# Kernel optimization log

Measured on AMD Instinct MI355X. Metric: run time of the kernel, lower is better.

The kernel has to match this reference:

```python
import jax, jax.numpy as jnp
import numpy as np

N_A = N_B = N_C = 50000
E = 800000
D_IN = 256
D_OUT = 128
T_ATT = 64


def _spmm(row, col, val, ft, n_dst):
    # sparse [n_dst, n_src] @ ft : gather src rows, scale, scatter-add to dst
    return jax.ops.segment_sum(val[:, None] * ft[col], row, num_segments=n_dst)


def setup_inputs() -> dict:
    key = jax.random.key(0)
    ks = jax.random.split(key, 40)
    f32 = jnp.float32
    inp = {
        'x_a': jax.random.normal(ks[0], (N_A, D_IN), f32),
        'x_b': jax.random.normal(ks[1], (N_B, D_IN), f32),
        'x_c': jax.random.normal(ks[2], (N_C, D_IN), f32),
    }
    # COO adjacency per relation: (dst_row, src_col, value)
    rel = {'ab': (N_A, N_B), 'ac': (N_A, N_C), 'ba': (N_B, N_A), 'ca': (N_C, N_A)}
    i = 3
    for name, (nd, ns) in rel.items():
        inp['row_' + name] = jax.random.randint(ks[i], (E,), 0, nd); i += 1
        inp['col_' + name] = jax.random.randint(ks[i], (E,), 0, ns); i += 1
        inp['val_' + name] = jax.random.uniform(ks[i], (E,), f32); i += 1
    # learned parameters (xavier-ish scale)
    def w(k, shape, s=0.05):
        return jax.random.normal(k, shape, f32) * s
    inp['w_self_a'] = w(ks[i], (D_IN, D_OUT)); i += 1
    inp['w_self_b'] = w(ks[i], (D_IN, D_OUT)); i += 1
    inp['w_self_c'] = w(ks[i], (D_IN, D_OUT)); i += 1
    inp['W_ab'] = w(ks[i], (D_IN, D_OUT)); i += 1
    inp['W_ac'] = w(ks[i], (D_IN, D_OUT)); i += 1
    inp['W_ba'] = w(ks[i], (D_IN, D_OUT)); i += 1
    inp['W_ca'] = w(ks[i], (D_IN, D_OUT)); i += 1
    inp['bias_a'] = w(ks[i], (1, D_OUT)); i += 1
    inp['bias_b'] = w(ks[i], (1, D_OUT)); i += 1
    inp['bias_c'] = w(ks[i], (1, D_OUT)); i += 1
    inp['w_cat_a'] = w(ks[i], (2 * D_OUT, D_OUT)); i += 1
    inp['w_cat_b'] = w(ks[i], (2 * D_OUT, D_OUT)); i += 1
    inp['w_cat_c'] = w(ks[i], (2 * D_OUT, D_OUT)); i += 1
    inp['w_query_a'] = w(ks[i], (D_OUT, T_ATT)); i += 1
    inp['w_keys_a'] = w(ks[i], (D_OUT, T_ATT)); i += 1
    inp['w_att_a'] = w(ks[i], (2 * T_ATT, 1)); i += 1
    return inp


def reference(x_a, x_b, x_c,
              row_ab, col_ab, val_ab, row_ac, col_ac, val_ac,
              row_ba, col_ba, val_ba, row_ca, col_ca, val_ca,
              w_self_a, w_self_b, w_self_c,
              W_ab, W_ac, W_ba, W_ca,
              bias_a, bias_b, bias_c,
              w_cat_a, w_cat_b, w_cat_c,
              w_query_a, w_keys_a, w_att_a):
    # ---- type 'a': neighbors [b, c], attention fusion ----
    self_a = x_a @ w_self_a                                   # [Na, D]
    nb_b = _spmm(row_ab, col_ab, val_ab, x_b @ W_ab, N_A)     # [Na, D]
    nb_c = _spmm(row_ac, col_ac, val_ac, x_c @ W_ac, N_A)     # [Na, D]
    q = self_a @ w_query_a                                    # [Na, T]
    e_b = jax.nn.elu(jnp.concatenate([nb_b @ w_keys_a, q], 1) @ w_att_a)  # [Na, 1]
    e_c = jax.nn.elu(jnp.concatenate([nb_c @ w_keys_a, q], 1) @ w_att_a)  # [Na, 1]
    att = jax.nn.softmax(jnp.concatenate([e_b, e_c], 1), axis=1)          # [Na, 2]
    agg_a = nb_b * att[:, :1] + nb_c * att[:, 1:2]
    out_a = jnp.concatenate([agg_a, self_a], 1) @ w_cat_a + bias_a
    # ---- type 'b': single neighbor 'a' ----
    self_b = x_b @ w_self_b
    agg_b = _spmm(row_ba, col_ba, val_ba, x_a @ W_ba, N_B)
    out_b = jnp.concatenate([agg_b, self_b], 1) @ w_cat_b + bias_b
    # ---- type 'c': single neighbor 'a' ----
    self_c = x_c @ w_self_c
    agg_c = _spmm(row_ca, col_ca, val_ca, x_a @ W_ca, N_C)
    out_c = jnp.concatenate([agg_c, self_c], 1) @ w_cat_c + bias_c
    # concat per-type outputs (all D_OUT wide) into one array
    return jnp.concatenate([out_a, out_b, out_c], 0)          # [Na+Nb+Nc, D]
```

## Files before the change

kernel.cpp:

```cpp
#include <hip/hip_runtime.h>

#define NA 50000
#define NE 800000
#define NBKT 196
#define CAP 4608
#define BSTRIDE (NBKT * CAP)

typedef unsigned int   u32;
typedef unsigned short u16;
typedef short s16x8 __attribute__((ext_vector_type(8)));
typedef float f32x4 __attribute__((ext_vector_type(4)));

__device__ __forceinline__ u16 f2bf(float f) {
  u32 u = __float_as_uint(f);
  u += 0x7fffu + ((u >> 16) & 1u);
  return (u16)(u >> 16);
}

__device__ __forceinline__ void acc8(float* a, uint4 q, float v) {
  a[0] += v * __uint_as_float(q.x << 16);
  a[1] += v * __uint_as_float(q.x & 0xffff0000u);
  a[2] += v * __uint_as_float(q.y << 16);
  a[3] += v * __uint_as_float(q.y & 0xffff0000u);
  a[4] += v * __uint_as_float(q.z << 16);
  a[5] += v * __uint_as_float(q.z & 0xffff0000u);
  a[6] += v * __uint_as_float(q.w << 16);
  a[7] += v * __uint_as_float(q.w & 0xffff0000u);
}

struct Rel4 { const int* row[4]; const int* col[4]; const float* val[4]; };

struct Prep {
  const float* src[10]; u16* dst[10];
  const float* wq; const float* wk; const float* wa; float* uvp;
  u32* gcur;
};

struct ConvArgs { const float* x[3]; u16* xb; };

struct FtArgs { const u16* A[3]; const u16* Bt[3]; u16* C[3]; };

__global__ __launch_bounds__(256) void k_prep(Prep P) {
  int gy = blockIdx.y;
  if (gy < 10) {
    int idx = blockIdx.x * 256 + threadIdx.x;
    int k = idx & 255, n = idx >> 8;
    P.dst[gy][n * 256 + k] = f2bf(P.src[gy][k * 128 + n]);
  } else if (blockIdx.x == 0) {
    int t = threadIdx.x;
    int d = t & 127, which = t >> 7;
    const float* w = which ? P.wq : P.wk;
    const float* a = P.wa + which * 64;
    float s = 0.f;
    for (int i = 0; i < 64; ++i) s += w[d * 64 + i] * a[i];
    P.uvp[which * 128 + d] = s;
  } else if (blockIdx.x == 1) {
    for (int i = threadIdx.x; i < 1024; i += 256)
      P.gcur[i] = (u32)((i & 255) * CAP);
  }
}

__global__ __launch_bounds__(256) void k_main1(Rel4 R, u32* __restrict__ gcur,
                                               uint2* __restrict__ pairs, ConvArgs CA) {
  __shared__ __align__(16) char smem[40960];
  const int gy = blockIdx.y;
  const int t = threadIdx.x;
  if (gy < 4) {
    if (blockIdx.x >= 196) return;
    int rel = gy;
    int e0 = blockIdx.x * 4096;
    int nrem = min(4096, NE - e0);
    u32* sw0  = (u32*)smem;
    u32* sval = sw0 + 4096;
    unsigned char* sbkt = (unsigned char*)(sval + 4096);
    u32* hist  = (u32*)(sbkt + 4096);
    u32* lscan = hist + 256;
    u32* cnt2  = lscan + 256;
    u32* gbase = cnt2 + 256;
    hist[t] = 0; cnt2[t] = 0;
    __syncthreads();
    const int* rr = R.row[rel];
    const int* cc = R.col[rel];
    const float* vl = R.val[rel];
    u32 w0[16]; u32 vv[16]; int bb[16];
    #pragma unroll
    for (int i = 0; i < 16; ++i) {
      int li = t + i * 256;
      bool ok = li < nrem;
      int idx = e0 + (ok ? li : 0);
      int r = ok ? rr[idx] : 0;
      int c = ok ? cc[idx] : 0;
      float v = ok ? vl[idx] : 0.f;
      u32 b = (u32)r >> 8;
      w0[i] = (u32)(c & 0xFFFF) | ((u32)(r & 255) << 16) | (b << 24);
      vv[i] = __float_as_uint(v);
      bb[i] = ok ? (int)b : -1;
      if (ok) atomicAdd(&hist[b], 1u);
    }
    __syncthreads();
    lscan[t] = hist[t];
    __syncthreads();
    for (int ofs = 1; ofs < 256; ofs <<= 1) {
      u32 y = (t >= ofs) ? lscan[t - ofs] : 0u;
      __syncthreads();
      lscan[t] += y;
      __syncthreads();
    }
    gbase[t] = atomicAdd(&gcur[rel * 256 + t], hist[t]);
    #pragma unroll
    for (int i = 0; i < 16; ++i) {
      if (bb[i] >= 0) {
        int b = bb[i];
        u32 p = (lscan[b] - hist[b]) + atomicAdd(&cnt2[b], 1u);
        sw0[p] = w0[i]; sval[p] = vv[i]; sbkt[p] = (unsigned char)b;
      }
    }
    __syncthreads();
    uint2* P = pairs + (size_t)rel * BSTRIDE;
    #pragma unroll
    for (int i = 0; i < 16; ++i) {
      int p = t + i * 256;
      if (p < nrem) {
        int b = sbkt[p];
        u32 gd = gbase[b] + (u32)p - (lscan[b] - hist[b]);
        uint2 pr; pr.x = sw0[p]; pr.y = sval[p];
        P[gd] = pr;
      }
    }
  } else {
    const size_t TOT = 38400000;
    const size_t TSZ = 12800000;
    size_t base = ((size_t)(gy - 4) * 391 + blockIdx.x) * 16384 + (size_t)t * 8;
    #pragma unroll
    for (int it = 0; it < 8; ++it) {
      size_t g = base + (size_t)it * 2048;
      if (g < TOT) {
        int which = (g >= 2 * TSZ) ? 2 : (g >= TSZ ? 1 : 0);
        size_t off = g - (size_t)which * TSZ;
        const float* sp = CA.x[which] + off;
        float4 v0 = *(const float4*)(sp);
        float4 v1 = *(const float4*)(sp + 4);
        s16x8 o;
        o[0] = (short)f2bf(v0.x); o[1] = (short)f2bf(v0.y);
        o[2] = (short)f2bf(v0.z); o[3] = (short)f2bf(v0.w);
        o[4] = (short)f2bf(v1.x); o[5] = (short)f2bf(v1.y);
        o[6] = (short)f2bf(v1.z); o[7] = (short)f2bf(v1.w);
        *(s16x8*)(CA.xb + g) = o;
      }
    }
  }
}

__global__ __launch_bounds__(256) void k_main2(const u32* __restrict__ gcur,
    int* __restrict__ ofs_s, int* __restrict__ ofs_e,
    const uint2* __restrict__ pairs, u32* __restrict__ epak, FtArgs Ar) {
  __shared__ __align__(16) char smem[40960];
  const int gy = blockIdx.y;
  const int t = threadIdx.x;
  if (gy < 4) {
    if (blockIdx.x >= 196) return;
    int rel = gy;
    int b = blockIdx.x;
    int base = b * CAP;
    int n = (int)gcur[rel * 256 + b] - base;
    u32* sw0  = (u32*)smem;
    u32* sv   = sw0 + CAP;
    u32* hist = sv + CAP;
    u32* scan = hist + 256;
    u32* cur  = scan + 256;
    hist[t] = 0;
    __syncthreads();
    const uint2* P = pairs + (size_t)rel * BSTRIDE;
    for (int p = t; p < n; p += 256) {
      uint2 pr = P[base + p];
      sw0[p] = pr.x; sv[p] = pr.y;
      atomicAdd(&hist[(pr.x >> 16) & 255], 1u);
    }
    __syncthreads();
    u32 own = hist[t];
    scan[t] = own;
    __syncthreads();
    for (int ofs = 1; ofs < 256; ofs <<= 1) {
      u32 y = (t >= ofs) ? scan[t - ofs] : 0u;
      __syncthreads();
      scan[t] += y;
      __syncthreads();
    }
    u32 excl = scan[t] - own;
    cur[t] = excl;
    int r0 = b << 8;
    if (r0 + t < NA) {
      ofs_s[(size_t)rel * NA + r0 + t] = base + (int)excl;
      ofs_e[(size_t)rel * NA + r0 + t] = base + (int)(excl + own);
    }
    __syncthreads();
    u32* E = epak + (size_t)rel * BSTRIDE;
    for (int p = t; p < n; p += 256) {
      u32 w = sw0[p];
      int rl = (w >> 16) & 255;
      u32 d = atomicAdd(&cur[rl], 1u);
      E[base + (int)d] = (w & 0xFFFFu) | ((u32)f2bf(__uint_as_float(sv[p])) << 16);
    }
  } else {
    u16* Al = (u16*)smem;
    u16* Bl = Al + 128 * 72;
    const int by = gy - 4;
    const int which = (by < 3) ? 0 : (by < 5 ? 1 : 2);
    const int col0 = (by - (which == 0 ? 0 : (which == 1 ? 3 : 5))) * 128;
    const int ldc = (which == 0) ? 384 : 256;
    const u16* A = Ar.A[which];
    const u16* Bt = Ar.Bt[which] + (size_t)col0 * 256;
    u16* C = Ar.C[which] + col0;
    const int row0 = blockIdx.x * 128;
    const int w = t >> 6, l = t & 63;
    const int wr = (w >> 1) * 64, wc = (w & 1) * 64;
    const int sr = t >> 1, kb = (t & 1) * 32;
    f32x4 acc[4][4] = {};
    for (int kk = 0; kk < 4; ++kk) {
      if (row0 + sr < NA) {
        const u16* ap = A + (size_t)(row0 + sr) * 256 + kk * 64 + kb;
        #pragma unroll
        for (int h = 0; h < 4; ++h)
          *(s16x8*)&Al[sr * 72 + kb + h * 8] = *(const s16x8*)(ap + h * 8);
      } else {
        s16x8 z = {0,0,0,0,0,0,0,0};
        #pragma unroll
        for (int h = 0; h < 4; ++h) *(s16x8*)&Al[sr * 72 + kb + h * 8] = z;
      }
      {
        const u16* bp = Bt + (size_t)sr * 256 + kk * 64 + kb;
        #pragma unroll
        for (int h = 0; h < 4; ++h)
          *(s16x8*)&Bl[sr * 72 + kb + h * 8] = *(const s16x8*)(bp + h * 8);
      }
      __syncthreads();
      #pragma unroll
      for (int ks = 0; ks < 2; ++ks) {
        s16x8 af[4], bfr[4];
        #pragma unroll
        for (int i = 0; i < 4; ++i)
          af[i] = *(const s16x8*)&Al[(wr + i * 16 + (l & 15)) * 72 + ks * 32 + (l >> 4) * 8];
        #pragma unroll
        for (int j = 0; j < 4; ++j)
          bfr[j] = *(const s16x8*)&Bl[(wc + j * 16 + (l & 15)) * 72 + ks * 32 + (l >> 4) * 8];
        #pragma unroll
        for (int i = 0; i < 4; ++i)
          #pragma unroll
          for (int j = 0; j < 4; ++j)
            acc[i][j] = __builtin_amdgcn_mfma_f32_16x16x32_bf16(af[i], bfr[j], acc[i][j], 0, 0, 0);
      }
      __syncthreads();
    }
    #pragma unroll
    for (int i = 0; i < 4; ++i)
      #pragma unroll
      for (int j = 0; j < 4; ++j)
        #pragma unroll
        for (int q = 0; q < 4; ++q) {
          int r = row0 + wr + i * 16 + (l >> 4) * 4 + q;
          if (r < NA) C[(size_t)r * ldc + wc + j * 16 + (l & 15)] = f2bf(acc[i][j][q]);
        }
  }
}

__global__ __launch_bounds__(256) void k_spmm(
    const int* __restrict__ ofs_s, const int* __restrict__ ofs_e,
    const u32* __restrict__ epak,
    const u16* __restrict__ ya, const u16* __restrict__ yb, const u16* __restrict__ yc,
    const float* __restrict__ uv,
    u16* __restrict__ agg_a, u16* __restrict__ agg_b, u16* __restrict__ agg_c) {
  int tid = threadIdx.x;
  int lane = tid & 63, wid = tid >> 6;
  int g = lane >> 4, gl = lane & 15;
  int row = blockIdx.x * 16 + wid * 4 + g;
  int gy = blockIdx.y;
  if (gy == 0) {
    float fb[8] = {0,0,0,0,0,0,0,0};
    float fc[8] = {0,0,0,0,0,0,0,0};
    {
      const u32* pr = epak;
      int i = ofs_s[row], e = ofs_e[row];
      for (; i + 4 <= e; i += 4) {
        u32 p0 = pr[i], p1 = pr[i + 1], p2 = pr[i + 2], p3 = pr[i + 3];
        uint4 q0 = *(const uint4*)((const u32*)(yb + (size_t)(p0 & 0xFFFFu) * 256) + gl * 4);
        uint4 q1 = *(const uint4*)((const u32*)(yb + (size_t)(p1 & 0xFFFFu) * 256) + gl * 4);
        uint4 q2 = *(const uint4*)((const u32*)(yb + (size_t)(p2 & 0xFFFFu) * 256) + gl * 4);
        uint4 q3 = *(const uint4*)((const u32*)(yb + (size_t)(p3 & 0xFFFFu) * 256) + gl * 4);
        acc8(fb, q0, __uint_as_float(p0 & 0xffff0000u));
        acc8(fb, q1, __uint_as_float(p1 & 0xffff0000u));
        acc8(fb, q2, __uint_as_float(p2 & 0xffff0000u));
        acc8(fb, q3, __uint_as_float(p3 & 0xffff0000u));
      }
      for (; i < e; ++i) {
        u32 p0 = pr[i];
        uint4 q0 = *(const uint4*)((const u32*)(yb + (size_t)(p0 & 0xFFFFu) * 256) + gl * 4);
        acc8(fb, q0, __uint_as_float(p0 & 0xffff0000u));
      }
    }
    {
      const u32* pr = epak + (size_t)BSTRIDE;
      int i = ofs_s[NA + row], e = ofs_e[NA + row];
      for (; i + 4 <= e; i += 4) {
        u32 p0 = pr[i], p1 = pr[i + 1], p2 = pr[i + 2], p3 = pr[i + 3];
        uint4 q0 = *(const uint4*)((const u32*)(yc + (size_t)(p0 & 0xFFFFu) * 256) + gl * 4);
        uint4 q1 = *(const uint4*)((const u32*)(yc + (size_t)(p1 & 0xFFFFu) * 256) + gl * 4);
        uint4 q2 = *(const uint4*)((const u32*)(yc + (size_t)(p2 & 0xFFFFu) * 256) + gl * 4);
        uint4 q3 = *(const uint4*)((const u32*)(yc + (size_t)(p3 & 0xFFFFu) * 256) + gl * 4);
        acc8(fc, q0, __uint_as_float(p0 & 0xffff0000u));
        acc8(fc, q1, __uint_as_float(p1 & 0xffff0000u));
        acc8(fc, q2, __uint_as_float(p2 & 0xffff0000u));
        acc8(fc, q3, __uint_as_float(p3 & 0xffff0000u));
      }
      for (; i < e; ++i) {
        u32 p0 = pr[i];
        uint4 q0 = *(const uint4*)((const u32*)(yc + (size_t)(p0 & 0xFFFFu) * 256) + gl * 4);
        acc8(fc, q0, __uint_as_float(p0 & 0xffff0000u));
      }
    }
    float sf[8];
    {
      uint4 sq = *(const uint4*)((const u32*)(ya + (size_t)row * 384) + gl * 4);
      sf[0] = __uint_as_float(sq.x << 16); sf[1] = __uint_as_float(sq.x & 0xffff0000u);
      sf[2] = __uint_as_float(sq.y << 16); sf[3] = __uint_as_float(sq.y & 0xffff0000u);
      sf[4] = __uint_as_float(sq.z << 16); sf[5] = __uint_as_float(sq.z & 0xffff0000u);
      sf[6] = __uint_as_float(sq.w << 16); sf[7] = __uint_as_float(sq.w & 0xffff0000u);
    }
    float pb = 0.f, pc = 0.f, pq = 0.f;
    const float* up = uv + gl * 8;
    const float* vp = uv + 128 + gl * 8;
    #pragma unroll
    for (int j = 0; j < 8; ++j) {
      pb += fb[j] * up[j];
      pc += fc[j] * up[j];
      pq += sf[j] * vp[j];
    }
    #pragma unroll
    for (int off = 1; off < 16; off <<= 1) {
      pb += __shfl_xor(pb, off);
      pc += __shfl_xor(pc, off);
      pq += __shfl_xor(pq, off);
    }
    float eb = pb + pq, ec = pc + pq;
    eb = eb > 0.f ? eb : (expf(eb) - 1.f);
    ec = ec > 0.f ? ec : (expf(ec) - 1.f);
    float m = fmaxf(eb, ec);
    float p0 = expf(eb - m), p1 = expf(ec - m);
    float inv = 1.f / (p0 + p1);
    float a0 = p0 * inv, a1 = p1 * inv;
    uint4 o;
    o.x = (u32)f2bf(a0 * fb[0] + a1 * fc[0]) | ((u32)f2bf(a0 * fb[1] + a1 * fc[1]) << 16);
    o.y = (u32)f2bf(a0 * fb[2] + a1 * fc[2]) | ((u32)f2bf(a0 * fb[3] + a1 * fc[3]) << 16);
    o.z = (u32)f2bf(a0 * fb[4] + a1 * fc[4]) | ((u32)f2bf(a0 * fb[5] + a1 * fc[5]) << 16);
    o.w = (u32)f2bf(a0 * fb[6] + a1 * fc[6]) | ((u32)f2bf(a0 * fb[7] + a1 * fc[7]) << 16);
    *(uint4*)((u32*)(agg_a + (size_t)row * 128) + gl * 4) = o;
  } else {
    int which = gy - 1;
    const int* os = ofs_s + (2 + which) * NA;
    const int* oe = ofs_e + (2 + which) * NA;
    const u32* pr = epak + (size_t)(2 + which) * BSTRIDE;
    const u16* ft = ya + (which ? 256 : 128);
    u16* agg = which ? agg_c : agg_b;
    float fa[8] = {0,0,0,0,0,0,0,0};
    int i = os[row], e = oe[row];
    for (; i + 4 <= e; i += 4) {
      u32 p0 = pr[i], p1 = pr[i + 1], p2 = pr[i + 2], p3 = pr[i + 3];
      uint4 q0 = *(const uint4*)((const u32*)(ft + (size_t)(p0 & 0xFFFFu) * 384) + gl * 4);
      uint4 q1 = *(const uint4*)((const u32*)(ft + (size_t)(p1 & 0xFFFFu) * 384) + gl * 4);
      uint4 q2 = *(const uint4*)((const u32*)(ft + (size_t)(p2 & 0xFFFFu) * 384) + gl * 4);
      uint4 q3 = *(const uint4*)((const u32*)(ft + (size_t)(p3 & 0xFFFFu) * 384) + gl * 4);
      acc8(fa, q0, __uint_as_float(p0 & 0xffff0000u));
      acc8(fa, q1, __uint_as_float(p1 & 0xffff0000u));
      acc8(fa, q2, __uint_as_float(p2 & 0xffff0000u));
      acc8(fa, q3, __uint_as_float(p3 & 0xffff0000u));
    }
    for (; i < e; ++i) {
      u32 p0 = pr[i];
      uint4 q0 = *(const uint4*)((const u32*)(ft + (size_t)(p0 & 0xFFFFu) * 384) + gl * 4);
      acc8(fa, q0, __uint_as_float(p0 & 0xffff0000u));
    }
    uint4 o;
    o.x = (u32)f2bf(fa[0]) | ((u32)f2bf(fa[1]) << 16);
    o.y = (u32)f2bf(fa[2]) | ((u32)f2bf(fa[3]) << 16);
    o.z = (u32)f2bf(fa[4]) | ((u32)f2bf(fa[5]) << 16);
    o.w = (u32)f2bf(fa[6]) | ((u32)f2bf(fa[7]) << 16);
    *(uint4*)((u32*)(agg + (size_t)row * 128) + gl * 4) = o;
  }
}

struct OutArgs {
  const u16* Agg[3]; const u16* Self[3]; int lds_[3];
  const u16* Bt[3]; const float* bias[3]; float* Out[3];
};

__global__ __launch_bounds__(256) void k_gemm_out(OutArgs Ar) {
  __shared__ u16 Al[128 * 72];
  __shared__ u16 Bl[128 * 72];
  const int which = blockIdx.y;
  const u16* Agg = Ar.Agg[which];
  const u16* Self = Ar.Self[which];
  const int ldself = Ar.lds_[which];
  const u16* Bt = Ar.Bt[which];
  const float* bias = Ar.bias[which];
  float* Out = Ar.Out[which];
  const int row0 = blockIdx.x * 128;
  const int t = threadIdx.x;
  const int w = t >> 6, l = t & 63;
  const int wr = (w >> 1) * 64, wc = (w & 1) * 64;
  const int sr = t >> 1, kb = (t & 1) * 32;
  f32x4 acc[4][4] = {};
  for (int kk = 0; kk < 4; ++kk) {
    {
      const u16* sp = (kk < 2) ? (Agg + (size_t)(row0 + sr) * 128 + kk * 64 + kb)
                               : (Self + (size_t)(row0 + sr) * ldself + (kk - 2) * 64 + kb);
      if (row0 + sr < NA) {
        #pragma unroll
        for (int h = 0; h < 4; ++h)
          *(s16x8*)&Al[sr * 72 + kb + h * 8] = *(const s16x8*)(sp + h * 8);
      } else {
        s16x8 z = {0,0,0,0,0,0,0,0};
        #pragma unroll
        for (int h = 0; h < 4; ++h) *(s16x8*)&Al[sr * 72 + kb + h * 8] = z;
      }
    }
    {
      const u16* bp = Bt + (size_t)sr * 256 + kk * 64 + kb;
      #pragma unroll
      for (int h = 0; h < 4; ++h)
        *(s16x8*)&Bl[sr * 72 + kb + h * 8] = *(const s16x8*)(bp + h * 8);
    }
    __syncthreads();
    #pragma unroll
    for (int ks = 0; ks < 2; ++ks) {
      s16x8 af[4], bfr[4];
      #pragma unroll
      for (int i = 0; i < 4; ++i)
        af[i] = *(const s16x8*)&Al[(wr + i * 16 + (l & 15)) * 72 + ks * 32 + (l >> 4) * 8];
      #pragma unroll
      for (int j = 0; j < 4; ++j)
        bfr[j] = *(const s16x8*)&Bl[(wc + j * 16 + (l & 15)) * 72 + ks * 32 + (l >> 4) * 8];
      #pragma unroll
      for (int i = 0; i < 4; ++i)
        #pragma unroll
        for (int j = 0; j < 4; ++j)
          acc[i][j] = __builtin_amdgcn_mfma_f32_16x16x32_bf16(af[i], bfr[j], acc[i][j], 0, 0, 0);
    }
    __syncthreads();
  }
  #pragma unroll
  for (int i = 0; i < 4; ++i)
    #pragma unroll
    for (int j = 0; j < 4; ++j)
      #pragma unroll
      for (int q = 0; q < 4; ++q) {
        int r = row0 + wr + i * 16 + (l >> 4) * 4 + q;
        int c = wc + j * 16 + (l & 15);
        if (r < NA) Out[(size_t)r * 128 + c] = acc[i][j][q] + bias[c];
      }
}

extern "C" void kernel_launch(void* const* d_in, const int* in_sizes, int n_in,
                              void* d_out, int out_size, void* d_ws, size_t ws_size,
                              hipStream_t stream) {
  const float* x_a = (const float*)d_in[0];
  const float* x_b = (const float*)d_in[1];
  const float* x_c = (const float*)d_in[2];
  const int* row_ab = (const int*)d_in[3];
  const int* col_ab = (const int*)d_in[4];
  const float* val_ab = (const float*)d_in[5];
  const int* row_ac = (const int*)d_in[6];
  const int* col_ac = (const int*)d_in[7];
  const float* val_ac = (const float*)d_in[8];
  const int* row_ba = (const int*)d_in[9];
  const int* col_ba = (const int*)d_in[10];
  const float* val_ba = (const float*)d_in[11];
  const int* row_ca = (const int*)d_in[12];
  const int* col_ca = (const int*)d_in[13];
  const float* val_ca = (const float*)d_in[14];
  const float* w_self_a = (const float*)d_in[15];
  const float* w_self_b = (const float*)d_in[16];
  const float* w_self_c = (const float*)d_in[17];
  const float* W_ab = (const float*)d_in[18];
  const float* W_ac = (const float*)d_in[19];
  const float* W_ba = (const float*)d_in[20];
  const float* W_ca = (const float*)d_in[21];
  const float* bias_a = (const float*)d_in[22];
  const float* bias_b = (const float*)d_in[23];
  const float* bias_c = (const float*)d_in[24];
  const float* w_cat_a = (const float*)d_in[25];
  const float* w_cat_b = (const float*)d_in[26];
  const float* w_cat_c = (const float*)d_in[27];
  const float* w_query_a = (const float*)d_in[28];
  const float* w_keys_a = (const float*)d_in[29];
  const float* w_att_a = (const float*)d_in[30];

  float* out = (float*)d_out;

  char* ws = (char*)d_ws;
  size_t off_b = 0;
  auto walloc = [&](size_t bytes) {
    void* p = ws + off_b;
    off_b = (off_b + bytes + 255) & ~(size_t)255;
    return p;
  };
  u16* ya = (u16*)walloc((size_t)NA * 384 * 2);
  u16* yb = (u16*)walloc((size_t)NA * 256 * 2);
  u16* yc = (u16*)walloc((size_t)NA * 256 * 2);
  u16* agg_a = (u16*)walloc((size_t)NA * 128 * 2);
  u16* agg_b = (u16*)walloc((size_t)NA * 128 * 2);
  u16* agg_c = (u16*)walloc((size_t)NA * 128 * 2);
  int* ofs_s = (int*)walloc((size_t)4 * NA * 4);
  int* ofs_e = (int*)walloc((size_t)4 * NA * 4);
  u32* gcur = (u32*)walloc((size_t)4 * 256 * 4);
  uint2* pairs = (uint2*)walloc((size_t)4 * BSTRIDE * 8);
  u32* epak = (u32*)walloc((size_t)4 * BSTRIDE * 4);
  u16* Wa_t = (u16*)walloc((size_t)384 * 256 * 2);
  u16* Wb_t = (u16*)walloc((size_t)256 * 256 * 2);
  u16* Wc_t = (u16*)walloc((size_t)256 * 256 * 2);
  u16* Wcat_a = (u16*)walloc((size_t)128 * 256 * 2);
  u16* Wcat_b = (u16*)walloc((size_t)128 * 256 * 2);
  u16* Wcat_c = (u16*)walloc((size_t)128 * 256 * 2);
  float* uvbuf = (float*)walloc(256 * 4);
  u16* xb = (u16*)walloc((size_t)3 * NA * 256 * 2);

  Rel4 R;
  R.row[0] = row_ab; R.col[0] = col_ab; R.val[0] = val_ab;
  R.row[1] = row_ac; R.col[1] = col_ac; R.val[1] = val_ac;
  R.row[2] = row_ba; R.col[2] = col_ba; R.val[2] = val_ba;
  R.row[3] = row_ca; R.col[3] = col_ca; R.val[3] = val_ca;

  Prep P;
  P.src[0] = w_self_a; P.dst[0] = Wa_t;
  P.src[1] = W_ba;     P.dst[1] = Wa_t + 128 * 256;
  P.src[2] = W_ca;     P.dst[2] = Wa_t + 256 * 256;
  P.src[3] = W_ab;     P.dst[3] = Wb_t;
  P.src[4] = w_self_b; P.dst[4] = Wb_t + 128 * 256;
  P.src[5] = W_ac;     P.dst[5] = Wc_t;
  P.src[6] = w_self_c; P.dst[6] = Wc_t + 128 * 256;
  P.src[7] = w_cat_a;  P.dst[7] = Wcat_a;
  P.src[8] = w_cat_b;  P.dst[8] = Wcat_b;
  P.src[9] = w_cat_c;  P.dst[9] = Wcat_c;
  P.wq = w_query_a; P.wk = w_keys_a; P.wa = w_att_a; P.uvp = uvbuf;
  P.gcur = gcur;

  dim3 gp(128, 11);
  k_prep<<<gp, 256, 0, stream>>>(P);

  ConvArgs CA;
  CA.x[0] = x_a; CA.x[1] = x_b; CA.x[2] = x_c;
  CA.xb = xb;
  dim3 g1(391, 11);
  k_main1<<<g1, 256, 0, stream>>>(R, gcur, pairs, CA);

  FtArgs FA;
  FA.A[0] = xb; FA.A[1] = xb + (size_t)NA * 256; FA.A[2] = xb + (size_t)2 * NA * 256;
  FA.Bt[0] = Wa_t; FA.Bt[1] = Wb_t; FA.Bt[2] = Wc_t;
  FA.C[0] = ya; FA.C[1] = yb; FA.C[2] = yc;
  dim3 g2(391, 11);
  k_main2<<<g2, 256, 0, stream>>>(gcur, ofs_s, ofs_e, pairs, epak, FA);

  dim3 gs(3125, 3);
  k_spmm<<<gs, 256, 0, stream>>>(ofs_s, ofs_e, epak, ya, yb, yc, uvbuf,
                                 agg_a, agg_b, agg_c);

  OutArgs OA;
  OA.Agg[0] = agg_a; OA.Agg[1] = agg_b; OA.Agg[2] = agg_c;
  OA.Self[0] = ya; OA.Self[1] = yb + 128; OA.Self[2] = yc + 128;
  OA.lds_[0] = 384; OA.lds_[1] = 256; OA.lds_[2] = 256;
  OA.Bt[0] = Wcat_a; OA.Bt[1] = Wcat_b; OA.Bt[2] = Wcat_c;
  OA.bias[0] = bias_a; OA.bias[1] = bias_b; OA.bias[2] = bias_c;
  OA.Out[0] = out; OA.Out[1] = out + (size_t)NA * 128; OA.Out[2] = out + (size_t)NA * 128 * 2;
  dim3 go(391, 3);
  k_gemm_out<<<go, 256, 0, stream>>>(OA);
}
```

Measured before the change: 308.3 us.

## Fuse output concat-GEMM into SpMM epilogue with MFMA-fragment weight layout

The final concat+linear GEMM is folded into the SpMM kernel. Each block stages its 16 aggregated rows plus the matching self features in LDS, then runs a small MFMA GEMM against w_cat, with the weights pre-laid out in fragment order during prep. This removes the agg buffers, one kernel launch, and the round trip through global memory. In exchange each SpMM block does extra work, and the weight fragments are reloaded from global or L2 for every block.

```diff
diff --git a/kernel.cpp b/kernel.cpp
--- a/kernel.cpp
+++ b/kernel.cpp
@@ -40,12 +40,20 @@
 
 struct FtArgs { const u16* A[3]; const u16* Bt[3]; u16* C[3]; };
 
+struct FuseW { const u16* Wf[3]; const float* bias[3]; float* out[3]; };
+
 __global__ __launch_bounds__(256) void k_prep(Prep P) {
   int gy = blockIdx.y;
-  if (gy < 10) {
+  if (gy < 7) {
     int idx = blockIdx.x * 256 + threadIdx.x;
     int k = idx & 255, n = idx >> 8;
     P.dst[gy][n * 256 + k] = f2bf(P.src[gy][k * 128 + n]);
+  } else if (gy < 10) {
+    int idx = blockIdx.x * 256 + threadIdx.x;
+    int e = idx & 7, l = (idx >> 3) & 63, jj = (idx >> 9) & 7, ks = idx >> 12;
+    int n = jj * 16 + (l & 15);
+    int k = ks * 32 + ((l >> 4) * 8) + e;
+    P.dst[gy][idx] = f2bf(P.src[gy][k * 128 + n]);
   } else if (blockIdx.x == 0) {
     int t = threadIdx.x;
     int d = t & 127, which = t >> 7;
@@ -267,12 +275,13 @@
     const int* __restrict__ ofs_s, const int* __restrict__ ofs_e,
     const u32* __restrict__ epak,
     const u16* __restrict__ ya, const u16* __restrict__ yb, const u16* __restrict__ yc,
-    const float* __restrict__ uv,
-    u16* __restrict__ agg_a, u16* __restrict__ agg_b, u16* __restrict__ agg_c) {
+    const float* __restrict__ uv, FuseW FW) {
+  __shared__ u16 Asm[16 * 264];
   int tid = threadIdx.x;
   int lane = tid & 63, wid = tid >> 6;
   int g = lane >> 4, gl = lane & 15;
-  int row = blockIdx.x * 16 + wid * 4 + g;
+  int lr = wid * 4 + g;
+  int row = blockIdx.x * 16 + lr;
   int gy = blockIdx.y;
   if (gy == 0) {
     float fb[8] = {0,0,0,0,0,0,0,0};
@@ -317,14 +326,12 @@
         acc8(fc, q0, __uint_as_float(p0 & 0xffff0000u));
       }
     }
+    uint4 sq = *(const uint4*)((const u32*)(ya + (size_t)row * 384) + gl * 4);
     float sf[8];
-    {
-      uint4 sq = *(const uint4*)((const u32*)(ya + (size_t)row * 384) + gl * 4);
-      sf[0] = __uint_as_float(sq.x << 16); sf[1] = __uint_as_float(sq.x & 0xffff0000u);
-      sf[2] = __uint_as_float(sq.y << 16); sf[3] = __uint_as_float(sq.y & 0xffff0000u);
-      sf[4] = __uint_as_float(sq.z << 16); sf[5] = __uint_as_float(sq.z & 0xffff0000u);
-      sf[6] = __uint_as_float(sq.w << 16); sf[7] = __uint_as_float(sq.w & 0xffff0000u);
-    }
+    sf[0] = __uint_as_float(sq.x << 16); sf[1] = __uint_as_float(sq.x & 0xffff0000u);
+    sf[2] = __uint_as_float(sq.y << 16); sf[3] = __uint_as_float(sq.y & 0xffff0000u);
+    sf[4] = __uint_as_float(sq.z << 16); sf[5] = __uint_as_float(sq.z & 0xffff0000u);
+    sf[6] = __uint_as_float(sq.w << 16); sf[7] = __uint_as_float(sq.w & 0xffff0000u);
     float pb = 0.f, pc = 0.f, pq = 0.f;
     const float* up = uv + gl * 8;
     const float* vp = uv + 128 + gl * 8;
@@ -347,19 +354,18 @@
     float p0 = expf(eb - m), p1 = expf(ec - m);
     float inv = 1.f / (p0 + p1);
     float a0 = p0 * inv, a1 = p1 * inv;
-    uint4 o;
-    o.x = (u32)f2bf(a0 * fb[0] + a1 * fc[0]) | ((u32)f2bf(a0 * fb[1] + a1 * fc[1]) << 16);
-    o.y = (u32)f2bf(a0 * fb[2] + a1 * fc[2]) | ((u32)f2bf(a0 * fb[3] + a1 * fc[3]) << 16);
-    o.z = (u32)f2bf(a0 * fb[4] + a1 * fc[4]) | ((u32)f2bf(a0 * fb[5] + a1 * fc[5]) << 16);
-    o.w = (u32)f2bf(a0 * fb[6] + a1 * fc[6]) | ((u32)f2bf(a0 * fb[7] + a1 * fc[7]) << 16);
-    *(uint4*)((u32*)(agg_a + (size_t)row * 128) + gl * 4) = o;
+    s16x8 av;
+    #pragma unroll
+    for (int j = 0; j < 8; ++j) av[j] = (short)f2bf(a0 * fb[j] + a1 * fc[j]);
+    *(s16x8*)&Asm[lr * 264 + gl * 8] = av;
+    *(s16x8*)&Asm[lr * 264 + 128 + gl * 8] = *(s16x8*)&sq;
   } else {
     int which = gy - 1;
     const int* os = ofs_s + (2 + which) * NA;
     const int* oe = ofs_e + (2 + which) * NA;
     const u32* pr = epak + (size_t)(2 + which) * BSTRIDE;
     const u16* ft = ya + (which ? 256 : 128);
-    u16* agg = which ? agg_c : agg_b;
+    const u16* selfp = which ? yc : yb;
     float fa[8] = {0,0,0,0,0,0,0,0};
     int i = os[row], e = oe[row];
     for (; i + 4 <= e; i += 4) {
@@ -378,84 +384,35 @@
       uint4 q0 = *(const uint4*)((const u32*)(ft + (size_t)(p0 & 0xFFFFu) * 384) + gl * 4);
       acc8(fa, q0, __uint_as_float(p0 & 0xffff0000u));
     }
-    uint4 o;
-    o.x = (u32)f2bf(fa[0]) | ((u32)f2bf(fa[1]) << 16);
-    o.y = (u32)f2bf(fa[2]) | ((u32)f2bf(fa[3]) << 16);
-    o.z = (u32)f2bf(fa[4]) | ((u32)f2bf(fa[5]) << 16);
-    o.w = (u32)f2bf(fa[6]) | ((u32)f2bf(fa[7]) << 16);
-    *(uint4*)((u32*)(agg + (size_t)row * 128) + gl * 4) = o;
+    s16x8 av;
+    #pragma unroll
+    for (int j = 0; j < 8; ++j) av[j] = (short)f2bf(fa[j]);
+    *(s16x8*)&Asm[lr * 264 + gl * 8] = av;
+    *(s16x8*)&Asm[lr * 264 + 128 + gl * 8] =
+        *(const s16x8*)(selfp + (size_t)row * 256 + 128 + gl * 8);
   }
-}
-
-struct OutArgs {
-  const u16* Agg[3]; const u16* Self[3]; int lds_[3];
-  const u16* Bt[3]; const float* bias[3]; float* Out[3];
-};
-
-__global__ __launch_bounds__(256) void k_gemm_out(OutArgs Ar) {
-  __shared__ u16 Al[128 * 72];
-  __shared__ u16 Bl[128 * 72];
-  const int which = blockIdx.y;
-  const u16* Agg = Ar.Agg[which];
-  const u16* Self = Ar.Self[which];
-  const int ldself = Ar.lds_[which];
-  const u16* Bt = Ar.Bt[which];
-  const float* bias = Ar.bias[which];
-  float* Out = Ar.Out[which];
-  const int row0 = blockIdx.x * 128;
-  const int t = threadIdx.x;
-  const int w = t >> 6, l = t & 63;
-  const int wr = (w >> 1) * 64, wc = (w & 1) * 64;
-  const int sr = t >> 1, kb = (t & 1) * 32;
-  f32x4 acc[4][4] = {};
-  for (int kk = 0; kk < 4; ++kk) {
-    {
-      const u16* sp = (kk < 2) ? (Agg + (size_t)(row0 + sr) * 128 + kk * 64 + kb)
-                               : (Self + (size_t)(row0 + sr) * ldself + (kk - 2) * 64 + kb);
-      if (row0 + sr < NA) {
-        #pragma unroll
-        for (int h = 0; h < 4; ++h)
-          *(s16x8*)&Al[sr * 72 + kb + h * 8] = *(const s16x8*)(sp + h * 8);
-      } else {
-        s16x8 z = {0,0,0,0,0,0,0,0};
-        #pragma unroll
-        for (int h = 0; h < 4; ++h) *(s16x8*)&Al[sr * 72 + kb + h * 8] = z;
-      }
-    }
-    {
-      const u16* bp = Bt + (size_t)sr * 256 + kk * 64 + kb;
-      #pragma unroll
-      for (int h = 0; h < 4; ++h)
-        *(s16x8*)&Bl[sr * 72 + kb + h * 8] = *(const s16x8*)(bp + h * 8);
-    }
-    __syncthreads();
-    #pragma unroll
-    for (int ks = 0; ks < 2; ++ks) {
-      s16x8 af[4], bfr[4];
-      #pragma unroll
-      for (int i = 0; i < 4; ++i)
-        af[i] = *(const s16x8*)&Al[(wr + i * 16 + (l & 15)) * 72 + ks * 32 + (l >> 4) * 8];
-      #pragma unroll
-      for (int j = 0; j < 4; ++j)
-        bfr[j] = *(const s16x8*)&Bl[(wc + j * 16 + (l & 15)) * 72 + ks * 32 + (l >> 4) * 8];
-      #pragma unroll
-      for (int i = 0; i < 4; ++i)
-        #pragma unroll
-        for (int j = 0; j < 4; ++j)
-          acc[i][j] = __builtin_amdgcn_mfma_f32_16x16x32_bf16(af[i], bfr[j], acc[i][j], 0, 0, 0);
-    }
-    __syncthreads();
+  __syncthreads();
+  const u16* Wf = FW.Wf[gy];
+  const float* bias = FW.bias[gy];
+  float* outp = FW.out[gy];
+  const int j0 = wid * 2, j1 = wid * 2 + 1;
+  f32x4 acc0 = {0.f, 0.f, 0.f, 0.f}, acc1 = {0.f, 0.f, 0.f, 0.f};
+  #pragma unroll
+  for (int ks = 0; ks < 8; ++ks) {
+    s16x8 a = *(const s16x8*)&Asm[(lane & 15) * 264 + ks * 32 + (lane >> 4) * 8];
+    s16x8 b0 = *(const s16x8*)(Wf + ((size_t)(ks * 8 + j0) * 64 + lane) * 8);
+    s16x8 b1 = *(const s16x8*)(Wf + ((size_t)(ks * 8 + j1) * 64 + lane) * 8);
+    acc0 = __builtin_amdgcn_mfma_f32_16x16x32_bf16(a, b0, acc0, 0, 0, 0);
+    acc1 = __builtin_amdgcn_mfma_f32_16x16x32_bf16(a, b1, acc1, 0, 0, 0);
   }
+  const int c0 = j0 * 16 + (lane & 15), c1 = j1 * 16 + (lane & 15);
+  const float b0v = bias[c0], b1v = bias[c1];
+  const int rbase = blockIdx.x * 16 + (lane >> 4) * 4;
   #pragma unroll
-  for (int i = 0; i < 4; ++i)
-    #pragma unroll
-    for (int j = 0; j < 4; ++j)
-      #pragma unroll
-      for (int q = 0; q < 4; ++q) {
-        int r = row0 + wr + i * 16 + (l >> 4) * 4 + q;
-        int c = wc + j * 16 + (l & 15);
-        if (r < NA) Out[(size_t)r * 128 + c] = acc[i][j][q] + bias[c];
-      }
+  for (int q = 0; q < 4; ++q) {
+    outp[(size_t)(rbase + q) * 128 + c0] = acc0[q] + b0v;
+    outp[(size_t)(rbase + q) * 128 + c1] = acc1[q] + b1v;
+  }
 }
 
 extern "C" void kernel_launch(void* const* d_in, const int* in_sizes, int n_in,
@@ -505,9 +462,6 @@
   u16* ya = (u16*)walloc((size_t)NA * 384 * 2);
   u16* yb = (u16*)walloc((size_t)NA * 256 * 2);
   u16* yc = (u16*)walloc((size_t)NA * 256 * 2);
-  u16* agg_a = (u16*)walloc((size_t)NA * 128 * 2);
-  u16* agg_b = (u16*)walloc((size_t)NA * 128 * 2);
-  u16* agg_c = (u16*)walloc((size_t)NA * 128 * 2);
   int* ofs_s = (int*)walloc((size_t)4 * NA * 4);
   int* ofs_e = (int*)walloc((size_t)4 * NA * 4);
   u32* gcur = (u32*)walloc((size_t)4 * 256 * 4);
@@ -558,17 +512,10 @@
   dim3 g2(391, 11);
   k_main2<<<g2, 256, 0, stream>>>(gcur, ofs_s, ofs_e, pairs, epak, FA);
 
+  FuseW FW;
+  FW.Wf[0] = Wcat_a; FW.Wf[1] = Wcat_b; FW.Wf[2] = Wcat_c;
+  FW.bias[0] = bias_a; FW.bias[1] = bias_b; FW.bias[2] = bias_c;
+  FW.out[0] = out; FW.out[1] = out + (size_t)NA * 128; FW.out[2] = out + (size_t)NA * 128 * 2;
   dim3 gs(3125, 3);
-  k_spmm<<<gs, 256, 0, stream>>>(ofs_s, ofs_e, epak, ya, yb, yc, uvbuf,
-                                 agg_a, agg_b, agg_c);
-
-  OutArgs OA;
-  OA.Agg[0] = agg_a; OA.Agg[1] = agg_b; OA.Agg[2] = agg_c;
-  OA.Self[0] = ya; OA.Self[1] = yb + 128; OA.Self[2] = yc + 128;
-  OA.lds_[0] = 384; OA.lds_[1] = 256; OA.lds_[2] = 256;
-  OA.Bt[0] = Wcat_a; OA.Bt[1] = Wcat_b; OA.Bt[2] = Wcat_c;
-  OA.bias[0] = bias_a; OA.bias[1] = bias_b; OA.bias[2] = bias_c;
-  OA.Out[0] = out; OA.Out[1] = out + (size_t)NA * 128; OA.Out[2] = out + (size_t)NA * 128 * 2;
-  dim3 go(391, 3);
-  k_gemm_out<<<go, 256, 0, stream>>>(OA);
-}
+  k_spmm<<<gs, 256, 0, stream>>>(ofs_s, ofs_e, epak, ya, yb, yc, uvbuf, FW);
+}
```

New measurement: 279.3 us. -9.4%, faster.
